# Optimization experiments

Measured on AMD Instinct MI355X. Metric: run time of the kernel, lower is better.

The kernel has to match this reference:

```python
import jax, jax.numpy as jnp
import numpy as np


def setup_inputs() -> dict:
    key = jax.random.key(0)
    ks = jax.random.split(key, 8)
    b, m, e, d = 8, 4096, 2048, 128
    features = jax.random.normal(ks[0], (b, m, d), dtype=jnp.float32)
    # sparse-ish binary incidence matrix (nodes x hyperedges)
    inc_mat = (jax.random.uniform(ks[1], (b, m, e)) < 0.02).astype(jnp.float32)
    s = 1.0 / np.sqrt(d)
    return {
        "features": features,
        "inc_mat": inc_mat,
        "vc_Wa": jax.random.uniform(ks[2], (d, d), minval=-s, maxval=s),
        "vc_Wp": jax.random.uniform(ks[3], (d, d), minval=-s, maxval=s),
        "vc_alpha": jnp.float32(0.5),
        "ec_Wa": jax.random.uniform(ks[4], (d, d), minval=-s, maxval=s),
        "ec_Wp": jax.random.uniform(ks[5], (d, d), minval=-s, maxval=s),
        "ec_alpha": jnp.float32(0.5),
        "n_layers": 3,
    }


def _vertex_conv(feat, inc, Wa, Wp, alpha, prev=None):
    # feat: [b,m,d], inc: [b,m,e]
    att = feat @ Wa.T                                   # [b,m,d]
    e_att = jnp.einsum('bme,bmd->bed', inc, att)        # inc^T @ att
    attw = jax.nn.softmax(e_att, axis=1)                # softmax over edges
    agg = jnp.einsum('bme,bmd->bed', inc, feat)         # collapsed bmed outer-product + contract
    ef = (agg * attw) @ Wp.T                            # [b,e,d]
    if prev is not None:
        ef = alpha * prev + (1.0 - alpha) * ef
    return ef


def _edge_conv(inc, edge_feats, Wa, Wp, alpha, prev=None):
    # NOTE: original EdgeConv computes softmax attention_weights but never uses them (dead code).
    w = jnp.einsum('bed,bme->bmd', edge_feats, inc)     # inc @ edge_feats
    nf = w @ Wp.T                                       # [b,m,d]
    if prev is not None:
        nf = alpha * prev + (1.0 - alpha) * nf
    return nf


def reference(features, inc_mat, vc_Wa, vc_Wp, vc_alpha, ec_Wa, ec_Wp, ec_alpha, n_layers):
    edge_feats = _vertex_conv(features, inc_mat, vc_Wa, vc_Wp, vc_alpha)
    node_feats = _edge_conv(inc_mat, edge_feats, ec_Wa, ec_Wp, ec_alpha)
    for _ in range(1, n_layers):
        edge_feats = _vertex_conv(features, inc_mat, vc_Wa, vc_Wp, vc_alpha, prev=edge_feats)
        node_feats = _edge_conv(inc_mat, edge_feats, ec_Wa, ec_Wp, ec_alpha, prev=node_feats)
    return node_feats, edge_feats
```

## Files before the change

kernel.cpp:

```cpp
#include <hip/hip_runtime.h>

#define BB 8
#define MM 4096
#define EE 2048
#define DD 128

typedef _Float16 f16x8 __attribute__((ext_vector_type(8)));
typedef float    f32x4 __attribute__((ext_vector_type(4)));

__global__ __launch_bounds__(256) void transpose_to16(const float* __restrict__ src,
                                                      _Float16* __restrict__ dst,
                                                      int R, int C)
{
    __shared__ alignas(16) float tile[64 * 67];
    const int tilesC = C >> 6;
    const int r0 = (blockIdx.x / tilesC) << 6;
    const int c0 = (blockIdx.x % tilesC) << 6;
    const float* s = src + (size_t)blockIdx.y * R * C;
    _Float16*   d = dst + (size_t)blockIdx.y * R * C;
    const int t = threadIdx.x;
    #pragma unroll
    for (int i = 0; i < 4; i++){
        int idx = t + 256 * i;
        int r = idx >> 4, c4 = idx & 15;
        float4 v = *(const float4*)(s + (size_t)(r0 + r) * C + c0 + c4 * 4);
        tile[(c4 * 4 + 0) * 67 + r] = v.x;
        tile[(c4 * 4 + 1) * 67 + r] = v.y;
        tile[(c4 * 4 + 2) * 67 + r] = v.z;
        tile[(c4 * 4 + 3) * 67 + r] = v.w;
    }
    __syncthreads();
    #pragma unroll
    for (int i = 0; i < 2; i++){
        int idx = t + 256 * i;
        int row = idx >> 3, rb = idx & 7;
        f16x8 h;
        #pragma unroll
        for (int j = 0; j < 8; j++) h[j] = (_Float16)tile[row * 67 + rb * 8 + j];
        *(f16x8*)(d + (size_t)(c0 + row) * R + r0 + rb * 8) = h;
    }
}

__global__ __launch_bounds__(256, 1) void fused_gemm1(const float* __restrict__ inc,
                                                      const _Float16* __restrict__ featT,
                                                      unsigned long long* __restrict__ bitsX,
                                                      float* __restrict__ p)
{
    __shared__ alignas(16) char smem[36864];

    const int x = blockIdx.x;
    const int b = blockIdx.y;
    const int z = blockIdx.z;
    const int t = threadIdx.x, lane = t & 63, w = t >> 6;
    const int fr = lane & 15, q = lane >> 4, q8 = q * 8;

    const int e0 = x * 256;
    const int ew0 = e0 + w * 64;
    const _Float16* dp = featT + (size_t)b * 128 * MM;
    const float* ip = inc + (size_t)b * MM * EE + ew0 + lane;
    unsigned long long* bxp = bitsX + ((size_t)b * 32 + (x * 4 + w)) * MM;

    f32x4 acc[4][8] = {};
    uint4 rd[4];
    float val[64];

    auto loadg = [&](int k0){
        #pragma unroll
        for (int i = 0; i < 4; i++){
            int idx = t + 256 * i;
            int dd = idx >> 3, kb = idx & 7;
            rd[i] = *(const uint4*)(dp + (size_t)dd * MM + k0 + kb * 8);
        }
        const float* rp = ip + (size_t)k0 * EE;
        #pragma unroll
        for (int j = 0; j < 64; j++) val[j] = rp[(size_t)j * EE];
    };
    auto stage = [&](int buf, int k0){
        _Float16* lD = (_Float16*)(smem + buf * 16384);
        unsigned long long* lBits = (unsigned long long*)(smem + 32768 + buf * 2048);
        #pragma unroll
        for (int i = 0; i < 4; i++){
            int idx = t + 256 * i;
            int dd = idx >> 3, kb = idx & 7;
            *(uint4*)&lD[dd * 64 + ((kb ^ (dd & 7)) * 8)] = rd[i];
        }
        unsigned long long wbits = 0;
        #pragma unroll
        for (int j = 0; j < 64; j++){
            unsigned long long bal = __ballot(val[j] != 0.0f);
            wbits = (lane == j) ? bal : wbits;
        }
        bxp[k0 + lane] = wbits;
        unsigned long long wT = 0;
        #pragma unroll
        for (int ei = 0; ei < 64; ei++){
            unsigned long long bal = __ballot((wbits >> ei) & 1ull);
            wT = (lane == ei) ? bal : wT;
        }
        lBits[w * 64 + lane] = wT;
    };
    auto compute = [&](int buf){
        const _Float16* lD = (const _Float16*)(smem + buf * 16384);
        const uint2* lBits = (const uint2*)(smem + 32768 + buf * 2048);
        uint2 bw[4];
        f16x8 af[4][2];
        #pragma unroll
        for (int s = 0; s < 4; s++) bw[s] = lBits[w * 64 + s * 16 + fr];
        #pragma unroll
        for (int s = 0; s < 4; s++)
            #pragma unroll
            for (int h = 0; h < 2; h++){
                unsigned word = h ? bw[s].y : bw[s].x;
                unsigned byte = (word >> q8) & 0xFFu;
                #pragma unroll
                for (int j = 0; j < 8; j++)
                    af[s][h][j] = ((byte >> j) & 1u) ? (_Float16)1.0f : (_Float16)0.0f;
            }
        #pragma unroll
        for (int h = 0; h < 2; h++)
            #pragma unroll
            for (int c = 0; c < 8; c++){
                int drow = c * 16 + fr;
                f16x8 bf = *(const f16x8*)&lD[drow * 64 + (((h * 4 + q) ^ (drow & 7)) * 8)];
                #pragma unroll
                for (int s = 0; s < 4; s++)
                    acc[s][c] = __builtin_amdgcn_mfma_f32_16x16x32_f16(af[s][h], bf, acc[s][c], 0, 0, 0);
            }
    };

    const int kbase = z * 1024;
    loadg(kbase); stage(0, kbase); __syncthreads();
    for (int c = 0; c < 16; c++){
        if (c + 1 < 16) loadg(kbase + (c + 1) * 64);
        compute(c & 1);
        if (c + 1 < 16) stage((c + 1) & 1, kbase + (c + 1) * 64);
        __syncthreads();
    }

    float* sT = (float*)smem;
    float* op = p + (size_t)z * 2097152 + ((size_t)b * EE + e0) * 128;
    for (int ph = 0; ph < 4; ph++){
        __syncthreads();
        if (w == ph){
            #pragma unroll
            for (int s = 0; s < 4; s++)
                #pragma unroll
                for (int c = 0; c < 8; c++)
                    #pragma unroll
                    for (int reg = 0; reg < 4; reg++)
                        sT[(s * 16 + q * 4 + reg) * 132 + c * 16 + fr] = acc[s][c][reg];
        }
        __syncthreads();
        #pragma unroll
        for (int i = 0; i < 8; i++){
            int idx = t + 256 * i;
            int lrow = idx >> 5, c4 = idx & 31;
            float4 v = *(const float4*)&sT[lrow * 132 + c4 * 4];
            *(float4*)(op + (size_t)(ph * 64 + lrow) * 128 + c4 * 4) = v;
        }
    }
}

__global__ __launch_bounds__(256) void bitgemm2_fused(const unsigned long long* __restrict__ bitsX,
                                                      const _Float16* __restrict__ PT,
                                                      const _Float16* __restrict__ Wc16,
                                                      float* __restrict__ node)
{
    __shared__ alignas(16) char smem[67584];
    const int b = blockIdx.y;
    const int m0 = blockIdx.x * 128;
    const unsigned long long* bxp = bitsX + (size_t)b * 32 * MM;
    const _Float16* dp = PT + (size_t)b * 128 * EE;
    float* op = node + ((size_t)b * MM + m0) * 128;

    const int t = threadIdx.x, lane = t & 63, w = t >> 6;
    const int fr = lane & 15, q = lane >> 4, q8 = q * 8;

    _Float16* lWc = (_Float16*)(smem + 34816);
    #pragma unroll
    for (int i = 0; i < 8; i++){
        int idx = t + 256 * i;
        int n = idx >> 4, kb = idx & 15;
        *(uint4*)&lWc[n * 128 + ((kb ^ (n & 7)) * 8)] =
            *(const uint4*)(Wc16 + (size_t)n * 128 + kb * 8);
    }

    f32x4 acc[2][8] = {};
    uint4 rd[4];
    unsigned long long rb;

    auto loadg = [&](int kg){
        #pragma unroll
        for (int i = 0; i < 4; i++){
            int idx = t + 256 * i;
            int dd = idx >> 3, kb = idx & 7;
            rd[i] = *(const uint4*)(dp + (size_t)dd * EE + kg + kb * 8);
        }
        if (t < 128) rb = bxp[(size_t)(kg >> 6) * MM + m0 + t];
    };
    auto stage = [&](int buf){
        _Float16* lD = (_Float16*)(smem + buf * 16384);
        unsigned long long* lB = (unsigned long long*)(smem + 32768 + buf * 1024);
        #pragma unroll
        for (int i = 0; i < 4; i++){
            int idx = t + 256 * i;
            int dd = idx >> 3, kb = idx & 7;
            *(uint4*)&lD[dd * 64 + ((kb ^ (dd & 7)) * 8)] = rd[i];
        }
        if (t < 128) lB[t] = rb;
    };
    auto compute = [&](int buf){
        const _Float16* lD = (const _Float16*)(smem + buf * 16384);
        const uint2* lB = (const uint2*)(smem + 32768 + buf * 1024);
        uint2 bw0 = lB[w * 32 + fr];
        uint2 bw1 = lB[w * 32 + 16 + fr];
        #pragma unroll
        for (int h = 0; h < 2; h++){
            unsigned word0 = h ? bw0.y : bw0.x;
            unsigned word1 = h ? bw1.y : bw1.x;
            unsigned byte0 = (word0 >> q8) & 0xFFu;
            unsigned byte1 = (word1 >> q8) & 0xFFu;
            f16x8 af0, af1;
            #pragma unroll
            for (int j = 0; j < 8; j++){
                af0[j] = ((byte0 >> j) & 1u) ? (_Float16)1.0f : (_Float16)0.0f;
                af1[j] = ((byte1 >> j) & 1u) ? (_Float16)1.0f : (_Float16)0.0f;
            }
            #pragma unroll
            for (int c = 0; c < 8; c++){
                int drow = c * 16 + fr;
                f16x8 bf = *(const f16x8*)&lD[drow * 64 + (((h * 4 + q) ^ (drow & 7)) * 8)];
                acc[0][c] = __builtin_amdgcn_mfma_f32_16x16x32_f16(af0, bf, acc[0][c], 0, 0, 0);
                acc[1][c] = __builtin_amdgcn_mfma_f32_16x16x32_f16(af1, bf, acc[1][c], 0, 0, 0);
            }
        }
    };

    loadg(0); stage(0); __syncthreads();
    for (int c = 0; c < 32; c++){
        if (c + 1 < 32) loadg((c + 1) * 64);
        compute(c & 1);
        if (c + 1 < 32) stage((c + 1) & 1);
        __syncthreads();
    }

    _Float16* sQ = (_Float16*)smem;
    #pragma unroll
    for (int u = 0; u < 2; u++)
        #pragma unroll
        for (int c = 0; c < 8; c++)
            #pragma unroll
            for (int reg = 0; reg < 4; reg++){
                int row = w * 32 + u * 16 + q * 4 + reg;
                int col = c * 16 + fr;
                sQ[row * 128 + (((col >> 3) ^ (row & 7)) * 8) + (col & 7)] = (_Float16)acc[u][c][reg];
            }
    f32x4 acc2[2][8] = {};
    #pragma unroll
    for (int kk = 0; kk < 4; kk++){
        int arow0 = w * 32 + fr;
        int arow1 = w * 32 + 16 + fr;
        f16x8 a20 = *(const f16x8*)&sQ[arow0 * 128 + (((kk * 4 + q) ^ (arow0 & 7)) * 8)];
        f16x8 a21 = *(const f16x8*)&sQ[arow1 * 128 + (((kk * 4 + q) ^ (arow1 & 7)) * 8)];
        #pragma unroll
        for (int c = 0; c < 8; c++){
            int n = c * 16 + fr;
            f16x8 b2 = *(const f16x8*)&lWc[n * 128 + (((kk * 4 + q) ^ (n & 7)) * 8)];
            acc2[0][c] = __builtin_amdgcn_mfma_f32_16x16x32_f16(a20, b2, acc2[0][c], 0, 0, 0);
            acc2[1][c] = __builtin_amdgcn_mfma_f32_16x16x32_f16(a21, b2, acc2[1][c], 0, 0, 0);
        }
    }
    __syncthreads();
    float* sD = (float*)smem;
    #pragma unroll
    for (int u = 0; u < 2; u++)
        #pragma unroll
        for (int c = 0; c < 8; c++)
            #pragma unroll
            for (int reg = 0; reg < 4; reg++)
                sD[(w * 32 + u * 16 + q * 4 + reg) * 132 + c * 16 + fr] = acc2[u][c][reg];
    __syncthreads();
    #pragma unroll
    for (int i = 0; i < 16; i++){
        int idx = t + 256 * i;
        int lrow = idx >> 5, c4 = idx & 31;
        float4 v = *(const float4*)&sD[lrow * 132 + c4 * 4];
        *(float4*)(op + (size_t)lrow * 128 + c4 * 4) = v;
    }
}

__global__ __launch_bounds__(256) void rowmm_sum4(const float* __restrict__ p,
                                                  const float* __restrict__ W,
                                                  float* aggOut,
                                                  float* __restrict__ C)
{
    __shared__ alignas(16) float lA[64][132];
    __shared__ alignas(16) float lW[64][132];
    const int t = threadIdx.x;
    const int row0 = blockIdx.x * 64;
    const float4* P4 = (const float4*)p;
    const float4* W4 = (const float4*)W;
    float4* A4 = (float4*)aggOut;
    const size_t SS = 2097152 / 4;

    #pragma unroll
    for (int i = 0; i < 8; i++){
        int idx = t + 256 * i;
        int r = idx >> 5, k4 = idx & 31;
        size_t gi = (size_t)(row0 + r) * 32 + k4;
        float4 a = P4[gi], b = P4[gi + SS], c = P4[gi + 2 * SS], d = P4[gi + 3 * SS];
        float4 s = make_float4(a.x + b.x + c.x + d.x, a.y + b.y + c.y + d.y,
                               a.z + b.z + c.z + d.z, a.w + b.w + c.w + d.w);
        *(float4*)&lA[r][((k4 ^ (r >> 3)) & 31) * 4] = s;
        A4[gi] = s;
    }
    const int rr = t >> 4, cg = t & 15;
    const int keyA = rr >> 1, keyW = cg >> 1;

    #pragma unroll
    for (int ph = 0; ph < 2; ph++){
        __syncthreads();
        #pragma unroll
        for (int i = 0; i < 8; i++){
            int idx = t + 256 * i;
            int cN = idx >> 5, k4 = idx & 31;
            *(float4*)&lW[cN][((k4 ^ (cN >> 3)) & 31) * 4] = W4[(size_t)(ph * 64 + cN) * 32 + k4];
        }
        __syncthreads();
        float s[4][4] = {};
        for (int k4 = 0; k4 < 32; k4++){
            float4 wv[4];
            #pragma unroll
            for (int jc = 0; jc < 4; jc++)
                wv[jc] = *(const float4*)&lW[cg * 4 + jc][((k4 ^ keyW) & 31) * 4];
            #pragma unroll
            for (int i = 0; i < 4; i++){
                float4 a = *(const float4*)&lA[rr * 4 + i][((k4 ^ keyA) & 31) * 4];
                #pragma unroll
                for (int jc = 0; jc < 4; jc++)
                    s[i][jc] += a.x * wv[jc].x + a.y * wv[jc].y + a.z * wv[jc].z + a.w * wv[jc].w;
            }
        }
        #pragma unroll
        for (int i = 0; i < 4; i++)
            *(float4*)&C[(size_t)(row0 + rr * 4 + i) * DD + ph * 64 + cg * 4] =
                make_float4(s[i][0], s[i][1], s[i][2], s[i][3]);
    }
}

__global__ __launch_bounds__(256) void rowmm(const float* A,
                                             const float* __restrict__ W,
                                             float* C)
{
    __shared__ alignas(16) float lA[64][132];
    __shared__ alignas(16) float lW[64][132];
    const int t = threadIdx.x;
    const int row0 = blockIdx.x * 64;
    const float4* A4 = (const float4*)A;
    const float4* W4 = (const float4*)W;

    #pragma unroll
    for (int i = 0; i < 8; i++){
        int idx = t + 256 * i;
        int r = idx >> 5, k4 = idx & 31;
        *(float4*)&lA[r][((k4 ^ (r >> 3)) & 31) * 4] = A4[(size_t)(row0 + r) * 32 + k4];
    }
    const int rr = t >> 4, cg = t & 15;
    const int keyA = rr >> 1, keyW = cg >> 1;

    #pragma unroll
    for (int ph = 0; ph < 2; ph++){
        __syncthreads();
        #pragma unroll
        for (int i = 0; i < 8; i++){
            int idx = t + 256 * i;
            int cN = idx >> 5, k4 = idx & 31;
            *(float4*)&lW[cN][((k4 ^ (cN >> 3)) & 31) * 4] = W4[(size_t)(ph * 64 + cN) * 32 + k4];
        }
        __syncthreads();
        float s[4][4] = {};
        for (int k4 = 0; k4 < 32; k4++){
            float4 wv[4];
            #pragma unroll
            for (int jc = 0; jc < 4; jc++)
                wv[jc] = *(const float4*)&lW[cg * 4 + jc][((k4 ^ keyW) & 31) * 4];
            #pragma unroll
            for (int i = 0; i < 4; i++){
                float4 a = *(const float4*)&lA[rr * 4 + i][((k4 ^ keyA) & 31) * 4];
                #pragma unroll
                for (int jc = 0; jc < 4; jc++)
                    s[i][jc] += a.x * wv[jc].x + a.y * wv[jc].y + a.z * wv[jc].z + a.w * wv[jc].w;
            }
        }
        #pragma unroll
        for (int i = 0; i < 4; i++)
            *(float4*)&C[(size_t)(row0 + rr * 4 + i) * DD + ph * 64 + cg * 4] =
                make_float4(s[i][0], s[i][1], s[i][2], s[i][3]);
    }
}

__global__ __launch_bounds__(256) void wc_mm16(const float* __restrict__ eWp,
                                               const float* __restrict__ vWp,
                                               _Float16* __restrict__ Wc16)
{
    int i = blockIdx.x * 2 + (threadIdx.x >> 7);
    int j = threadIdx.x & 127;
    float acc = 0.f;
    for (int k = 0; k < 128; k++)
        acc += eWp[i * 128 + k] * vWp[k * 128 + j];
    Wc16[i * 128 + j] = (_Float16)acc;
}

__global__ __launch_bounds__(256) void sm_part(const float* __restrict__ eatt,
                                               float* __restrict__ part)
{
    const int b = blockIdx.x, slab = blockIdx.y;
    const int t = threadIdx.x;
    const int dl = t & 127, eh = t >> 7;
    const size_t base = (size_t)b * EE * DD + dl;
    const int e0 = slab * 128;
    float v[64];
    #pragma unroll
    for (int s = 0; s < 64; s++)
        v[s] = eatt[base + (size_t)(e0 + eh + 2 * s) * DD];
    float m = -1e30f;
    #pragma unroll
    for (int s = 0; s < 64; s++) m = fmaxf(m, v[s]);
    float l = 0.f;
    #pragma unroll
    for (int s = 0; s < 64; s++) l += __expf(v[s] - m);
    __shared__ float red[2][128][2];
    red[eh][dl][0] = m; red[eh][dl][1] = l;
    __syncthreads();
    if (t < 128){
        float m0 = red[0][t][0], l0 = red[0][t][1];
        float m1 = red[1][t][0], l1 = red[1][t][1];
        float M = fmaxf(m0, m1);
        float L = l0 * __expf(m0 - M) + l1 * __expf(m1 - M);
        float* pp = part + ((size_t)(b * 16 + slab) * DD + t) * 2;
        pp[0] = M; pp[1] = L;
    }
}

__global__ __launch_bounds__(256) void sm_apply(float* __restrict__ eatt,
                                                const float* __restrict__ agg,
                                                const float* __restrict__ part)
{
    const int b = blockIdx.x, sl = blockIdx.y;
    const int t = threadIdx.x;
    __shared__ float mv[128], iv[128];
    if (t < 128){
        float mbuf[16], lbuf[16];
        float M = -1e30f;
        #pragma unroll
        for (int s = 0; s < 16; s++){
            const float* pp = part + ((size_t)(b * 16 + s) * DD + t) * 2;
            mbuf[s] = pp[0]; lbuf[s] = pp[1];
            M = fmaxf(M, mbuf[s]);
        }
        float L = 0.f;
        #pragma unroll
        for (int s = 0; s < 16; s++) L += lbuf[s] * __expf(mbuf[s] - M);
        mv[t] = M; iv[t] = 1.f / L;
    }
    __syncthreads();
    const int dl = t & 127, eh = t >> 7;
    const size_t base = (size_t)b * EE * DD + dl;
    const int e0 = sl * 128;
    for (int s = 0; s < 64; s++){
        size_t ix = base + (size_t)(e0 + eh + 2 * s) * DD;
        eatt[ix] = agg[ix] * __expf(eatt[ix] - mv[dl]) * iv[dl];
    }
}

extern "C" void kernel_launch(void* const* d_in, const int* in_sizes, int n_in,
                              void* d_out, int out_size, void* d_ws, size_t ws_size,
                              hipStream_t stream)
{
    const float* feat = (const float*)d_in[0];
    const float* inc  = (const float*)d_in[1];
    const float* vWa  = (const float*)d_in[2];
    const float* vWp  = (const float*)d_in[3];
    const float* eWp  = (const float*)d_in[6];

    float* node_out = (float*)d_out;
    float* edge_out = node_out + (size_t)BB * MM * DD;

    char* w = (char*)d_ws;
    unsigned long long* bitsX = (unsigned long long*)w;
    float* pk  = (float*)(w + ((size_t)8 << 20));
    float* agg = pk;
    _Float16* PT = (_Float16*)(w + ((size_t)16 << 20));
    _Float16* Wc16 = (_Float16*)(w + ((size_t)40 << 20));

    _Float16* featT = (_Float16*)node_out;
    float* eattP = node_out + 2097152;
    float* part  = edge_out;

    dim3 blk(256);

    transpose_to16<<<dim3((MM / 64) * (DD / 64), BB), blk, 0, stream>>>(feat, featT, MM, DD);
    wc_mm16<<<dim3(64), blk, 0, stream>>>(eWp, vWp, Wc16);
    fused_gemm1<<<dim3(EE / 256, BB, 4), blk, 0, stream>>>(inc, featT, bitsX, pk);
    rowmm_sum4<<<dim3(BB * EE / 64), blk, 0, stream>>>(pk, vWa, agg, eattP);
    sm_part <<<dim3(BB, 16), blk, 0, stream>>>(eattP, part);
    sm_apply<<<dim3(BB, 16), blk, 0, stream>>>(eattP, agg, part);
    rowmm<<<dim3(BB * EE / 64), blk, 0, stream>>>(eattP, vWp, edge_out);
    transpose_to16<<<dim3((EE / 64) * (DD / 64), BB), blk, 0, stream>>>(eattP, PT, EE, DD);
    bitgemm2_fused<<<dim3(MM / 128, BB), blk, 0, stream>>>(bitsX, PT, Wc16, node_out);
}
```

Baseline: 529.1 us.

## Fuse softmax stats, softmax apply, projection and transpose; merge prep kernels; remap block IDs

Per-column softmax max and sum are now computed inside the attention projection kernel, replacing a separate partial-softmax pass. Softmax normalization, the Wp projection and the fp16 transpose into PT are folded into one kernel. The feature transpose and the weight-product kernel are merged into a single launch. Block indices in the GEMM kernels are remapped to a flat grid, which changes scheduling and cache locality. The aim is fewer launches and fewer global round trips over the edge tensors, at the cost of extra syncs and a serial 32-partition merge per block.

```diff
diff --git a/kernel.cpp b/kernel.cpp
--- a/kernel.cpp
+++ b/kernel.cpp
@@ -8,22 +8,33 @@
 typedef _Float16 f16x8 __attribute__((ext_vector_type(8)));
 typedef float    f32x4 __attribute__((ext_vector_type(4)));
 
-__global__ __launch_bounds__(256) void transpose_to16(const float* __restrict__ src,
-                                                      _Float16* __restrict__ dst,
-                                                      int R, int C)
+__global__ __launch_bounds__(256) void prep(const float* __restrict__ feat,
+                                            _Float16* __restrict__ featT,
+                                            const float* __restrict__ eWp,
+                                            const float* __restrict__ vWp,
+                                            _Float16* __restrict__ Wc16)
 {
     __shared__ alignas(16) float tile[64 * 67];
-    const int tilesC = C >> 6;
-    const int r0 = (blockIdx.x / tilesC) << 6;
-    const int c0 = (blockIdx.x % tilesC) << 6;
-    const float* s = src + (size_t)blockIdx.y * R * C;
-    _Float16*   d = dst + (size_t)blockIdx.y * R * C;
     const int t = threadIdx.x;
+    if (blockIdx.x >= 1024){
+        int i = (blockIdx.x - 1024) * 2 + (t >> 7);
+        int j = t & 127;
+        float acc = 0.f;
+        for (int k = 0; k < 128; k++)
+            acc += eWp[i * 128 + k] * vWp[k * 128 + j];
+        Wc16[i * 128 + j] = (_Float16)acc;
+        return;
+    }
+    const int b = blockIdx.x >> 7, tl = blockIdx.x & 127;
+    const int r0 = (tl >> 1) << 6;
+    const int c0 = (tl & 1) << 6;
+    const float* s = feat + (size_t)b * MM * DD;
+    _Float16*   d = featT + (size_t)b * MM * DD;
     #pragma unroll
     for (int i = 0; i < 4; i++){
         int idx = t + 256 * i;
         int r = idx >> 4, c4 = idx & 15;
-        float4 v = *(const float4*)(s + (size_t)(r0 + r) * C + c0 + c4 * 4);
+        float4 v = *(const float4*)(s + (size_t)(r0 + r) * DD + c0 + c4 * 4);
         tile[(c4 * 4 + 0) * 67 + r] = v.x;
         tile[(c4 * 4 + 1) * 67 + r] = v.y;
         tile[(c4 * 4 + 2) * 67 + r] = v.z;
@@ -37,7 +48,7 @@
         f16x8 h;
         #pragma unroll
         for (int j = 0; j < 8; j++) h[j] = (_Float16)tile[row * 67 + rb * 8 + j];
-        *(f16x8*)(d + (size_t)(c0 + row) * R + r0 + rb * 8) = h;
+        *(f16x8*)(d + (size_t)(c0 + row) * MM + r0 + rb * 8) = h;
     }
 }
 
@@ -48,9 +59,12 @@
 {
     __shared__ alignas(16) char smem[36864];
 
-    const int x = blockIdx.x;
-    const int b = blockIdx.y;
-    const int z = blockIdx.z;
+    const int id = blockIdx.x;
+    const int s_ = id >> 3;
+    const int x  = s_ & 7;
+    const int pair = (id & 7) * 4 + (s_ >> 3);
+    const int b = pair & 7, z = pair >> 3;
+
     const int t = threadIdx.x, lane = t & 63, w = t >> 6;
     const int fr = lane & 15, q = lane >> 4, q8 = q * 8;
 
@@ -161,141 +175,16 @@
     }
 }
 
-__global__ __launch_bounds__(256) void bitgemm2_fused(const unsigned long long* __restrict__ bitsX,
-                                                      const _Float16* __restrict__ PT,
-                                                      const _Float16* __restrict__ Wc16,
-                                                      float* __restrict__ node)
-{
-    __shared__ alignas(16) char smem[67584];
-    const int b = blockIdx.y;
-    const int m0 = blockIdx.x * 128;
-    const unsigned long long* bxp = bitsX + (size_t)b * 32 * MM;
-    const _Float16* dp = PT + (size_t)b * 128 * EE;
-    float* op = node + ((size_t)b * MM + m0) * 128;
-
-    const int t = threadIdx.x, lane = t & 63, w = t >> 6;
-    const int fr = lane & 15, q = lane >> 4, q8 = q * 8;
-
-    _Float16* lWc = (_Float16*)(smem + 34816);
-    #pragma unroll
-    for (int i = 0; i < 8; i++){
-        int idx = t + 256 * i;
-        int n = idx >> 4, kb = idx & 15;
-        *(uint4*)&lWc[n * 128 + ((kb ^ (n & 7)) * 8)] =
-            *(const uint4*)(Wc16 + (size_t)n * 128 + kb * 8);
-    }
-
-    f32x4 acc[2][8] = {};
-    uint4 rd[4];
-    unsigned long long rb;
-
-    auto loadg = [&](int kg){
-        #pragma unroll
-        for (int i = 0; i < 4; i++){
-            int idx = t + 256 * i;
-            int dd = idx >> 3, kb = idx & 7;
-            rd[i] = *(const uint4*)(dp + (size_t)dd * EE + kg + kb * 8);
-        }
-        if (t < 128) rb = bxp[(size_t)(kg >> 6) * MM + m0 + t];
-    };
-    auto stage = [&](int buf){
-        _Float16* lD = (_Float16*)(smem + buf * 16384);
-        unsigned long long* lB = (unsigned long long*)(smem + 32768 + buf * 1024);
-        #pragma unroll
-        for (int i = 0; i < 4; i++){
-            int idx = t + 256 * i;
-            int dd = idx >> 3, kb = idx & 7;
-            *(uint4*)&lD[dd * 64 + ((kb ^ (dd & 7)) * 8)] = rd[i];
-        }
-        if (t < 128) lB[t] = rb;
-    };
-    auto compute = [&](int buf){
-        const _Float16* lD = (const _Float16*)(smem + buf * 16384);
-        const uint2* lB = (const uint2*)(smem + 32768 + buf * 1024);
-        uint2 bw0 = lB[w * 32 + fr];
-        uint2 bw1 = lB[w * 32 + 16 + fr];
-        #pragma unroll
-        for (int h = 0; h < 2; h++){
-            unsigned word0 = h ? bw0.y : bw0.x;
-            unsigned word1 = h ? bw1.y : bw1.x;
-            unsigned byte0 = (word0 >> q8) & 0xFFu;
-            unsigned byte1 = (word1 >> q8) & 0xFFu;
-            f16x8 af0, af1;
-            #pragma unroll
-            for (int j = 0; j < 8; j++){
-                af0[j] = ((byte0 >> j) & 1u) ? (_Float16)1.0f : (_Float16)0.0f;
-                af1[j] = ((byte1 >> j) & 1u) ? (_Float16)1.0f : (_Float16)0.0f;
-            }
-            #pragma unroll
-            for (int c = 0; c < 8; c++){
-                int drow = c * 16 + fr;
-                f16x8 bf = *(const f16x8*)&lD[drow * 64 + (((h * 4 + q) ^ (drow & 7)) * 8)];
-                acc[0][c] = __builtin_amdgcn_mfma_f32_16x16x32_f16(af0, bf, acc[0][c], 0, 0, 0);
-                acc[1][c] = __builtin_amdgcn_mfma_f32_16x16x32_f16(af1, bf, acc[1][c], 0, 0, 0);
-            }
-        }
-    };
-
-    loadg(0); stage(0); __syncthreads();
-    for (int c = 0; c < 32; c++){
-        if (c + 1 < 32) loadg((c + 1) * 64);
-        compute(c & 1);
-        if (c + 1 < 32) stage((c + 1) & 1);
-        __syncthreads();
-    }
-
-    _Float16* sQ = (_Float16*)smem;
-    #pragma unroll
-    for (int u = 0; u < 2; u++)
-        #pragma unroll
-        for (int c = 0; c < 8; c++)
-            #pragma unroll
-            for (int reg = 0; reg < 4; reg++){
-                int row = w * 32 + u * 16 + q * 4 + reg;
-                int col = c * 16 + fr;
-                sQ[row * 128 + (((col >> 3) ^ (row & 7)) * 8) + (col & 7)] = (_Float16)acc[u][c][reg];
-            }
-    f32x4 acc2[2][8] = {};
-    #pragma unroll
-    for (int kk = 0; kk < 4; kk++){
-        int arow0 = w * 32 + fr;
-        int arow1 = w * 32 + 16 + fr;
-        f16x8 a20 = *(const f16x8*)&sQ[arow0 * 128 + (((kk * 4 + q) ^ (arow0 & 7)) * 8)];
-        f16x8 a21 = *(const f16x8*)&sQ[arow1 * 128 + (((kk * 4 + q) ^ (arow1 & 7)) * 8)];
-        #pragma unroll
-        for (int c = 0; c < 8; c++){
-            int n = c * 16 + fr;
-            f16x8 b2 = *(const f16x8*)&lWc[n * 128 + (((kk * 4 + q) ^ (n & 7)) * 8)];
-            acc2[0][c] = __builtin_amdgcn_mfma_f32_16x16x32_f16(a20, b2, acc2[0][c], 0, 0, 0);
-            acc2[1][c] = __builtin_amdgcn_mfma_f32_16x16x32_f16(a21, b2, acc2[1][c], 0, 0, 0);
-        }
-    }
-    __syncthreads();
-    float* sD = (float*)smem;
-    #pragma unroll
-    for (int u = 0; u < 2; u++)
-        #pragma unroll
-        for (int c = 0; c < 8; c++)
-            #pragma unroll
-            for (int reg = 0; reg < 4; reg++)
-                sD[(w * 32 + u * 16 + q * 4 + reg) * 132 + c * 16 + fr] = acc2[u][c][reg];
-    __syncthreads();
-    #pragma unroll
-    for (int i = 0; i < 16; i++){
-        int idx = t + 256 * i;
-        int lrow = idx >> 5, c4 = idx & 31;
-        float4 v = *(const float4*)&sD[lrow * 132 + c4 * 4];
-        *(float4*)(op + (size_t)lrow * 128 + c4 * 4) = v;
-    }
-}
-
-__global__ __launch_bounds__(256) void rowmm_sum4(const float* __restrict__ p,
-                                                  const float* __restrict__ W,
-                                                  float* aggOut,
-                                                  float* __restrict__ C)
+__global__ __launch_bounds__(256) void rowmm_sum4_sm(const float* __restrict__ p,
+                                                     const float* __restrict__ W,
+                                                     float* aggOut,
+                                                     float* __restrict__ C,
+                                                     float* __restrict__ part)
 {
     __shared__ alignas(16) float lA[64][132];
     __shared__ alignas(16) float lW[64][132];
+    __shared__ alignas(16) float red[16][64];
+    __shared__ alignas(16) float colm[64];
     const int t = threadIdx.x;
     const int row0 = blockIdx.x * 64;
     const float4* P4 = (const float4*)p;
@@ -345,29 +234,110 @@
         for (int i = 0; i < 4; i++)
             *(float4*)&C[(size_t)(row0 + rr * 4 + i) * DD + ph * 64 + cg * 4] =
                 make_float4(s[i][0], s[i][1], s[i][2], s[i][3]);
+
+        {
+            float4 mt = make_float4(
+                fmaxf(fmaxf(s[0][0], s[1][0]), fmaxf(s[2][0], s[3][0])),
+                fmaxf(fmaxf(s[0][1], s[1][1]), fmaxf(s[2][1], s[3][1])),
+                fmaxf(fmaxf(s[0][2], s[1][2]), fmaxf(s[2][2], s[3][2])),
+                fmaxf(fmaxf(s[0][3], s[1][3]), fmaxf(s[2][3], s[3][3])));
+            *(float4*)&red[rr][cg * 4] = mt;
+        }
+        __syncthreads();
+        if (t < 64){
+            float m = -1e30f;
+            #pragma unroll
+            for (int r2 = 0; r2 < 16; r2++) m = fmaxf(m, red[r2][t]);
+            colm[t] = m;
+        }
+        __syncthreads();
+        {
+            float4 cm = *(const float4*)&colm[cg * 4];
+            float4 st;
+            st.x = __expf(s[0][0]-cm.x) + __expf(s[1][0]-cm.x) + __expf(s[2][0]-cm.x) + __expf(s[3][0]-cm.x);
+            st.y = __expf(s[0][1]-cm.y) + __expf(s[1][1]-cm.y) + __expf(s[2][1]-cm.y) + __expf(s[3][1]-cm.y);
+            st.z = __expf(s[0][2]-cm.z) + __expf(s[1][2]-cm.z) + __expf(s[2][2]-cm.z) + __expf(s[3][2]-cm.z);
+            st.w = __expf(s[0][3]-cm.w) + __expf(s[1][3]-cm.w) + __expf(s[2][3]-cm.w) + __expf(s[3][3]-cm.w);
+            *(float4*)&red[rr][cg * 4] = st;
+        }
+        __syncthreads();
+        if (t < 64){
+            float l = 0.f;
+            #pragma unroll
+            for (int r2 = 0; r2 < 16; r2++) l += red[r2][t];
+            float* pp = part + ((size_t)blockIdx.x * 128 + ph * 64 + t) * 2;
+            pp[0] = colm[t]; pp[1] = l;
+        }
     }
 }
 
-__global__ __launch_bounds__(256) void rowmm(const float* A,
-                                             const float* __restrict__ W,
-                                             float* C)
+__global__ __launch_bounds__(256) void apply_edge_pt(const float* __restrict__ eatt,
+                                                     const float* __restrict__ agg,
+                                                     const float* __restrict__ part,
+                                                     const float* __restrict__ W,
+                                                     float* __restrict__ edge,
+                                                     _Float16* __restrict__ PT)
 {
     __shared__ alignas(16) float lA[64][132];
     __shared__ alignas(16) float lW[64][132];
+    __shared__ alignas(16) float mv[128];
+    __shared__ alignas(16) float iv[128];
     const int t = threadIdx.x;
-    const int row0 = blockIdx.x * 64;
-    const float4* A4 = (const float4*)A;
-    const float4* W4 = (const float4*)W;
-
+    const int b = blockIdx.x >> 5;
+    const int sl = blockIdx.x & 31;
+    const int e0g = sl * 64;
+
+    if (t < 128){
+        float M = -1e30f, L = 0.f;
+        for (int s = 0; s < 32; s++){
+            const float* pp = part + ((size_t)(b * 32 + s) * 128 + t) * 2;
+            float m = pp[0], l = pp[1];
+            float nM = fmaxf(M, m);
+            L = L * __expf(M - nM) + l * __expf(m - nM);
+            M = nM;
+        }
+        mv[t] = M; iv[t] = 1.f / L;
+    }
+    __syncthreads();
+
+    const float4* AG4 = (const float4*)(agg  + ((size_t)b * EE + e0g) * DD);
+    const float4* ET4 = (const float4*)(eatt + ((size_t)b * EE + e0g) * DD);
+    const int k4c = t & 31;
+    float4 mv4 = *(const float4*)&mv[k4c * 4];
+    float4 iv4 = *(const float4*)&iv[k4c * 4];
     #pragma unroll
     for (int i = 0; i < 8; i++){
         int idx = t + 256 * i;
-        int r = idx >> 5, k4 = idx & 31;
-        *(float4*)&lA[r][((k4 ^ (r >> 3)) & 31) * 4] = A4[(size_t)(row0 + r) * 32 + k4];
-    }
+        int r = idx >> 5;
+        size_t gi = (size_t)r * 32 + k4c;
+        float4 av = AG4[gi], ev = ET4[gi];
+        float4 pv = make_float4(av.x * __expf(ev.x - mv4.x) * iv4.x,
+                                av.y * __expf(ev.y - mv4.y) * iv4.y,
+                                av.z * __expf(ev.z - mv4.z) * iv4.z,
+                                av.w * __expf(ev.w - mv4.w) * iv4.w);
+        *(float4*)&lA[r][((k4c ^ (r >> 3)) & 31) * 4] = pv;
+    }
+    __syncthreads();
+
+    {
+        int d = t >> 1, half = t & 1;
+        _Float16* pt = PT + (size_t)b * DD * EE + (size_t)d * EE + e0g + half * 32;
+        #pragma unroll
+        for (int g = 0; g < 4; g++){
+            f16x8 hv;
+            #pragma unroll
+            for (int j = 0; j < 8; j++){
+                int e = half * 32 + g * 8 + j;
+                hv[j] = (_Float16)lA[e][(((d >> 2) ^ (e >> 3)) & 31) * 4 + (d & 3)];
+            }
+            *(f16x8*)(pt + g * 8) = hv;
+        }
+    }
+
+    const float4* W4 = (const float4*)W;
     const int rr = t >> 4, cg = t & 15;
     const int keyA = rr >> 1, keyW = cg >> 1;
-
+    float* C = edge + ((size_t)b * EE + e0g) * DD;
     #pragma unroll
     for (int ph = 0; ph < 2; ph++){
         __syncthreads();
@@ -394,82 +364,136 @@
         }
         #pragma unroll
         for (int i = 0; i < 4; i++)
-            *(float4*)&C[(size_t)(row0 + rr * 4 + i) * DD + ph * 64 + cg * 4] =
+            *(float4*)&C[(size_t)(rr * 4 + i) * DD + ph * 64 + cg * 4] =
                 make_float4(s[i][0], s[i][1], s[i][2], s[i][3]);
     }
 }
 
-__global__ __launch_bounds__(256) void wc_mm16(const float* __restrict__ eWp,
-                                               const float* __restrict__ vWp,
-                                               _Float16* __restrict__ Wc16)
+__global__ __launch_bounds__(256) void bitgemm2_fused(const unsigned long long* __restrict__ bitsX,
+                                                      const _Float16* __restrict__ PT,
+                                                      const _Float16* __restrict__ Wc16,
+                                                      float* __restrict__ node)
 {
-    int i = blockIdx.x * 2 + (threadIdx.x >> 7);
-    int j = threadIdx.x & 127;
-    float acc = 0.f;
-    for (int k = 0; k < 128; k++)
-        acc += eWp[i * 128 + k] * vWp[k * 128 + j];
-    Wc16[i * 128 + j] = (_Float16)acc;
-}
-
-__global__ __launch_bounds__(256) void sm_part(const float* __restrict__ eatt,
-                                               float* __restrict__ part)
-{
-    const int b = blockIdx.x, slab = blockIdx.y;
-    const int t = threadIdx.x;
-    const int dl = t & 127, eh = t >> 7;
-    const size_t base = (size_t)b * EE * DD + dl;
-    const int e0 = slab * 128;
-    float v[64];
-    #pragma unroll
-    for (int s = 0; s < 64; s++)
-        v[s] = eatt[base + (size_t)(e0 + eh + 2 * s) * DD];
-    float m = -1e30f;
-    #pragma unroll
-    for (int s = 0; s < 64; s++) m = fmaxf(m, v[s]);
-    float l = 0.f;
-    #pragma unroll
-    for (int s = 0; s < 64; s++) l += __expf(v[s] - m);
-    __shared__ float red[2][128][2];
-    red[eh][dl][0] = m; red[eh][dl][1] = l;
+    __shared__ alignas(16) char smem[67584];
+    const int b = blockIdx.x & 7;
+    const int m0 = (blockIdx.x >> 3) * 128;
+    const unsigned long long* bxp = bitsX + (size_t)b * 32 * MM;
+    const _Float16* dp = PT + (size_t)b * 128 * EE;
+    float* op = node + ((size_t)b * MM + m0) * 128;
+
+    const int t = threadIdx.x, lane = t & 63, w = t >> 6;
+    const int fr = lane & 15, q = lane >> 4, q8 = q * 8;
+
+    _Float16* lWc = (_Float16*)(smem + 34816);
+    #pragma unroll
+    for (int i = 0; i < 8; i++){
+        int idx = t + 256 * i;
+        int n = idx >> 4, kb = idx & 15;
+        *(uint4*)&lWc[n * 128 + ((kb ^ (n & 7)) * 8)] =
+            *(const uint4*)(Wc16 + (size_t)n * 128 + kb * 8);
+    }
+
+    f32x4 acc[2][8] = {};
+    uint4 rd[4];
+    unsigned long long rb;
+
+    auto loadg = [&](int kg){
+        #pragma unroll
+        for (int i = 0; i < 4; i++){
+            int idx = t + 256 * i;
+            int dd = idx >> 3, kb = idx & 7;
+            rd[i] = *(const uint4*)(dp + (size_t)dd * EE + kg + kb * 8);
+        }
+        if (t < 128) rb = bxp[(size_t)(kg >> 6) * MM + m0 + t];
+    };
+    auto stage = [&](int buf){
+        _Float16* lD = (_Float16*)(smem + buf * 16384);
+        unsigned long long* lB = (unsigned long long*)(smem + 32768 + buf * 1024);
+        #pragma unroll
+        for (int i = 0; i < 4; i++){
+            int idx = t + 256 * i;
+            int dd = idx >> 3, kb = idx & 7;
+            *(uint4*)&lD[dd * 64 + ((kb ^ (dd & 7)) * 8)] = rd[i];
+        }
+        if (t < 128) lB[t] = rb;
+    };
+    auto compute = [&](int buf){
+        const _Float16* lD = (const _Float16*)(smem + buf * 16384);
+        const uint2* lB = (const uint2*)(smem + 32768 + buf * 1024);
+        uint2 bw0 = lB[w * 32 + fr];
+        uint2 bw1 = lB[w * 32 + 16 + fr];
+        #pragma unroll
+        for (int h = 0; h < 2; h++){
+            unsigned word0 = h ? bw0.y : bw0.x;
+            unsigned word1 = h ? bw1.y : bw1.x;
+            unsigned byte0 = (word0 >> q8) & 0xFFu;
+            unsigned byte1 = (word1 >> q8) & 0xFFu;
+            f16x8 af0, af1;
+            #pragma unroll
+            for (int j = 0; j < 8; j++){
+                af0[j] = ((byte0 >> j) & 1u) ? (_Float16)1.0f : (_Float16)0.0f;
+                af1[j] = ((byte1 >> j) & 1u) ? (_Float16)1.0f : (_Float16)0.0f;
+            }
+            #pragma unroll
+            for (int c = 0; c < 8; c++){
+                int drow = c * 16 + fr;
+                f16x8 bf = *(const f16x8*)&lD[drow * 64 + (((h * 4 + q) ^ (drow & 7)) * 8)];
+                acc[0][c] = __builtin_amdgcn_mfma_f32_16x16x32_f16(af0, bf, acc[0][c], 0, 0, 0);
+                acc[1][c] = __builtin_amdgcn_mfma_f32_16x16x32_f16(af1, bf, acc[1][c], 0, 0, 0);
+            }
+        }
+    };
+
+    loadg(0); stage(0); __syncthreads();
+    for (int c = 0; c < 32; c++){
+        if (c + 1 < 32) loadg((c + 1) * 64);
+        compute(c & 1);
+        if (c + 1 < 32) stage((c + 1) & 1);
+        __syncthreads();
+    }
+
+    _Float16* sQ = (_Float16*)smem;
+    #pragma unroll
+    for (int u = 0; u < 2; u++)
+        #pragma unroll
+        for (int c = 0; c < 8; c++)
+            #pragma unroll
+            for (int reg = 0; reg < 4; reg++){
+                int row = w * 32 + u * 16 + q * 4 + reg;
+                int col = c * 16 + fr;
+                sQ[row * 128 + (((col >> 3) ^ (row & 7)) * 8) + (col & 7)] = (_Float16)acc[u][c][reg];
+            }
+    f32x4 acc2[2][8] = {};
+    #pragma unroll
+    for (int kk = 0; kk < 4; kk++){
+        int arow0 = w * 32 + fr;
+        int arow1 = w * 32 + 16 + fr;
+        f16x8 a20 = *(const f16x8*)&sQ[arow0 * 128 + (((kk * 4 + q) ^ (arow0 & 7)) * 8)];
+        f16x8 a21 = *(const f16x8*)&sQ[arow1 * 128 + (((kk * 4 + q) ^ (arow1 & 7)) * 8)];
+        #pragma unroll
+        for (int c = 0; c < 8; c++){
+            int n = c * 16 + fr;
+            f16x8 b2 = *(const f16x8*)&lWc[n * 128 + (((kk * 4 + q) ^ (n & 7)) * 8)];
+            acc2[0][c] = __builtin_amdgcn_mfma_f32_16x16x32_f16(a20, b2, acc2[0][c], 0, 0, 0);
+            acc2[1][c] = __builtin_amdgcn_mfma_f32_16x16x32_f16(a21, b2, acc2[1][c], 0, 0, 0);
+        }
+    }
     __syncthreads();
-    if (t < 128){
-        float m0 = red[0][t][0], l0 = red[0][t][1];
-        float m1 = red[1][t][0], l1 = red[1][t][1];
-        float M = fmaxf(m0, m1);
-        float L = l0 * __expf(m0 - M) + l1 * __expf(m1 - M);
-        float* pp = part + ((size_t)(b * 16 + slab) * DD + t) * 2;
-        pp[0] = M; pp[1] = L;
-    }
-}
-
-__global__ __launch_bounds__(256) void sm_apply(float* __restrict__ eatt,
-                                                const float* __restrict__ agg,
-                                                const float* __restrict__ part)
-{
-    const int b = blockIdx.x, sl = blockIdx.y;
-    const int t = threadIdx.x;
-    __shared__ float mv[128], iv[128];
-    if (t < 128){
-        float mbuf[16], lbuf[16];
-        float M = -1e30f;
-        #pragma unroll
-        for (int s = 0; s < 16; s++){
-            const float* pp = part + ((size_t)(b * 16 + s) * DD + t) * 2;
-            mbuf[s] = pp[0]; lbuf[s] = pp[1];
-            M = fmaxf(M, mbuf[s]);
-        }
-        float L = 0.f;
-        #pragma unroll
-        for (int s = 0; s < 16; s++) L += lbuf[s] * __expf(mbuf[s] - M);
-        mv[t] = M; iv[t] = 1.f / L;
-    }
+    float* sD = (float*)smem;
+    #pragma unroll
+    for (int u = 0; u < 2; u++)
+        #pragma unroll
+        for (int c = 0; c < 8; c++)
+            #pragma unroll
+            for (int reg = 0; reg < 4; reg++)
+                sD[(w * 32 + u * 16 + q * 4 + reg) * 132 + c * 16 + fr] = acc2[u][c][reg];
     __syncthreads();
-    const int dl = t & 127, eh = t >> 7;
-    const size_t base = (size_t)b * EE * DD + dl;
-    const int e0 = sl * 128;
-    for (int s = 0; s < 64; s++){
-        size_t ix = base + (size_t)(e0 + eh + 2 * s) * DD;
-        eatt[ix] = agg[ix] * __expf(eatt[ix] - mv[dl]) * iv[dl];
+    #pragma unroll
+    for (int i = 0; i < 16; i++){
+        int idx = t + 256 * i;
+        int lrow = idx >> 5, c4 = idx & 31;
+        float4 v = *(const float4*)&sD[lrow * 132 + c4 * 4];
+        *(float4*)(op + (size_t)lrow * 128 + c4 * 4) = v;
     }
 }
 
@@ -492,20 +516,16 @@
     float* agg = pk;
     _Float16* PT = (_Float16*)(w + ((size_t)16 << 20));
     _Float16* Wc16 = (_Float16*)(w + ((size_t)40 << 20));
+    float* part = (float*)(w + ((size_t)41 << 20));
 
     _Float16* featT = (_Float16*)node_out;
     float* eattP = node_out + 2097152;
-    float* part  = edge_out;
 
     dim3 blk(256);
 
-    transpose_to16<<<dim3((MM / 64) * (DD / 64), BB), blk, 0, stream>>>(feat, featT, MM, DD);
-    wc_mm16<<<dim3(64), blk, 0, stream>>>(eWp, vWp, Wc16);
-    fused_gemm1<<<dim3(EE / 256, BB, 4), blk, 0, stream>>>(inc, featT, bitsX, pk);
-    rowmm_sum4<<<dim3(BB * EE / 64), blk, 0, stream>>>(pk, vWa, agg, eattP);
-    sm_part <<<dim3(BB, 16), blk, 0, stream>>>(eattP, part);
-    sm_apply<<<dim3(BB, 16), blk, 0, stream>>>(eattP, agg, part);
-    rowmm<<<dim3(BB * EE / 64), blk, 0, stream>>>(eattP, vWp, edge_out);
-    transpose_to16<<<dim3((EE / 64) * (DD / 64), BB), blk, 0, stream>>>(eattP, PT, EE, DD);
-    bitgemm2_fused<<<dim3(MM / 128, BB), blk, 0, stream>>>(bitsX, PT, Wc16, node_out);
+    prep<<<dim3(1088), blk, 0, stream>>>(feat, featT, eWp, vWp, Wc16);
+    fused_gemm1<<<dim3(256), blk, 0, stream>>>(inc, featT, bitsX, pk);
+    rowmm_sum4_sm<<<dim3(BB * EE / 64), blk, 0, stream>>>(pk, vWa, agg, eattP, part);
+    apply_edge_pt<<<dim3(256), blk, 0, stream>>>(eattP, agg, part, vWp, edge_out, PT);
+    bitgemm2_fused<<<dim3(256), blk, 0, stream>>>(bitsX, PT, Wc16, node_out);
 }
```

Measured after the change: 517.4 us, median of 2. -2.2%, faster.
